# Optimization experiments

Measured on AMD Instinct MI355X. Metric: run time of the kernel, lower is better.

## Reference

```python
import jax, jax.numpy as jnp
import numpy as np

# ---- forest structure (static) ----
B = 32                      # number of trees in the batch
DEPTH = 12                  # topological levels per tree
LEVELS = [2 ** d for d in range(DEPTH)]           # nodes per level (root=level 0)
STARTS = np.concatenate([[0], np.cumsum(LEVELS)[:-1]]).astype(int)
NPG = int(sum(LEVELS))      # 4095 nodes per graph, node 0 = root
N = B * NPG                 # 131040 total nodes
VOCAB = 20000               # dataset.PAD_TOKEN_VALUE + 1
PAD = VOCAB - 1             # padding_idx
E = 256                     # embedding_dim (x_size)
H = 256                     # lstm_output_dim (h_size)
C = 104                     # num_classes (extra_non_linear=None)


def setup_inputs() -> dict:
    key = jax.random.key(0)
    ks = jax.random.split(key, 8)
    # random parent in the previous level for every non-root node (irregular fan-in)
    rng = np.random.RandomState(0)
    par = np.full(N, -1, dtype=np.int64)
    for g in range(B):
        off = g * NPG
        for d in range(1, DEPTH):
            nd = LEVELS[d]
            par[off + STARTS[d]: off + STARTS[d] + nd] = (
                off + STARTS[d - 1] + rng.randint(0, LEVELS[d - 1], size=nd))
    s = 0.05
    return {
        'x': jax.random.randint(ks[0], (N,), 0, VOCAB),
        'par': jnp.asarray(par),
        'emb': jax.random.normal(ks[1], (VOCAB, E), jnp.float32) * s,
        'W_iou': jax.random.normal(ks[2], (3 * H, E), jnp.float32) * s,
        'U_iou': jax.random.normal(ks[3], (3 * H, H), jnp.float32) * s,
        'b_iou': jnp.zeros((1, 3 * H), jnp.float32),
        'U_f_w': jax.random.normal(ks[4], (H, H), jnp.float32) * s,
        'U_f_b': jnp.zeros((H,), jnp.float32),
        'lin_w': jax.random.normal(ks[5], (C, H), jnp.float32) * s,
        'lin_b': jnp.zeros((C,), jnp.float32),
    }


def _forward(x, par, emb, W_iou, U_iou, b_iou, U_f_w, U_f_b, lin_w, lin_b):
    emb = emb.at[PAD].set(0.0)                 # padding_idx row is zero
    x_vec = emb[x]                             # [N, E]
    iou = x_vec @ W_iou.T                      # [N, 3H], W_iou has no bias
    h = jnp.zeros((N, H), x_vec.dtype)
    c = jnp.zeros((N, H), x_vec.dtype)
    offs = jnp.arange(B) * NPG
    # topological propagation: leaves (deepest level) -> root, per generation
    for d in range(DEPTH - 1, -1, -1):
        nd = LEVELS[d]
        nids = (offs[:, None] + STARTS[d] + jnp.arange(nd)).reshape(-1)  # [B*nd]
        iou_n = iou[nids]
        if d < DEPTH - 1:
            nc = LEVELS[d + 1]
            cids = (offs[:, None] + STARTS[d + 1] + jnp.arange(nc)).reshape(-1)
            h_ch = h[cids]                     # mailbox gather of child states
            c_ch = c[cids]
            p = par[cids]                      # global parent id per child
            seg = (p // NPG) * nd + (p % NPG - STARTS[d])  # parent slot in this level
            f = jax.nn.sigmoid(h_ch @ U_f_w.T + U_f_b)     # per-child forget gate
            h_tild = jax.ops.segment_sum(h_ch, seg, num_segments=B * nd)
            c_agg = jax.ops.segment_sum(f * c_ch, seg, num_segments=B * nd)
            iou_n = iou_n + h_tild @ U_iou.T
            c_n = c_agg
        else:
            c_n = jnp.zeros((B * nd, H), x_vec.dtype)
        iou_n = iou_n + b_iou
        i, o, u = jnp.split(iou_n, 3, axis=1)
        c_new = jax.nn.sigmoid(i) * jnp.tanh(u) + c_n
        h_new = jax.nn.sigmoid(o) * jnp.tanh(c_new)
        h = h.at[nids].set(h_new)
        c = c.at[nids].set(c_new)
    roots = h[offs]                            # graph.ndata['h'][0] per graph
    return roots @ lin_w.T + lin_b             # [B, num_classes]


def reference(x, par, emb, W_iou, U_iou, b_iou, U_f_w, U_f_b, lin_w, lin_b):
    return _forward(x, par, emb, W_iou, U_iou, b_iou, U_f_w, U_f_b, lin_w, lin_b)
```

## Files before the change

kernel.cpp:

```cpp
#include <hip/hip_runtime.h>
#include <hip/hip_bf16.h>


#define B_G     32
#define NPG     4095
#define NTOT    (B_G * NPG)
#define NCLS    104
#define VOCAB   20000
#define PAD_TOK 19999
#define KCAP    24
#define LB(d)   (32 * ((1 << (d)) - 1))

typedef unsigned short u16;
typedef unsigned int   u32;
typedef __attribute__((ext_vector_type(8))) short bfrag8;
typedef __attribute__((ext_vector_type(4))) float ffrag4;

__device__ __forceinline__ float bf2f(u16 v) {
    union { u32 u; float f; } x; x.u = ((u32)v) << 16; return x.f;
}
__device__ __forceinline__ u16 f2bf(float f) {
    union { __hip_bfloat16 h; u16 u; } c; c.h = __float2bfloat16(f); return c.u;
}
__device__ __forceinline__ float loadv(const void* b, int i, int isf32) {
    return isf32 ? ((const float*)b)[i] : bf2f(((const u16*)b)[i]);
}
__device__ __forceinline__ float sigf(float x) { return 1.f / (1.f + __expf(-x)); }

__global__ void probe_kernel(const void* emb, const void* Wiou, const void* Uiou,
                             const void* Ufw, const void* lw,
                             const int* x32, const int* par32, int* flags)
{
    if (threadIdx.x != 0 || blockIdx.x != 0) return;
    const void* ptrs[5] = { emb, Wiou, Uiou, Ufw, lw };
    for (int i = 0; i < 5; ++i) {
        const u16* p = (const u16*)ptrs[i];
        int big = 0;
        for (int k = 0; k < 128; ++k) {
            u32 e = (((u32)p[k]) << 16 >> 23) & 0xFF;
            if (e >= 129) ++big;
        }
        flags[i] = (big >= 4) ? 1 : 0;
    }
    int zx = 1;
    for (int k = 1; k <= 15; k += 2) if (x32[k] != 0) zx = 0;
    flags[5] = zx;
    flags[6] = (par32[3] == 0 && par32[5] == 0) ? 1 : 0;
}

__global__ __launch_bounds__(256) void prep_kernel(
    const int* __restrict__ x, const int* __restrict__ par,
    int* __restrict__ tokLvl, int* __restrict__ cnt, int* __restrict__ bucket,
    const int* __restrict__ flags)
{
    int gid = blockIdx.x * 256 + threadIdx.x;
    if (gid >= NTOT) return;
    int g     = (int)((u32)gid / NPG);
    int local = gid - g * NPG;
    int v  = local + 1;
    int d  = 31 - __clz(v);
    int j  = local - ((1 << d) - 1);
    int tok = flags[5] ? x[2 * gid] : x[gid];
    if (tok < 0 || tok >= VOCAB) tok = PAD_TOK;
    tokLvl[LB(d) + (g << d) + j] = tok;
    if (local > 0) {
        int p  = flags[6] ? par[2 * gid] : par[gid];
        p = max(0, min(p, NTOT - 1));
        int pg = (int)((u32)p / NPG);
        int pl = p - pg * NPG;
        int pd = d - 1;
        int ps = LB(pd) + (pg << pd) + (pl - ((1 << pd) - 1));
        ps = max(0, min(ps, 65503));
        int slot = atomicAdd(&cnt[ps], 1);
        if (slot < KCAP) bucket[(size_t)ps * KCAP + slot] = (g << d) + j;
    }
}

__global__ __launch_bounds__(256) void embconv_kernel(
    const void* __restrict__ emb, u16* __restrict__ embb,
    const int* __restrict__ flags)
{
    int i8 = (blockIdx.x * 256 + threadIdx.x) * 8;
    if (i8 >= VOCAB * 256) return;
    u16 v[8];
    if ((i8 >> 8) == PAD_TOK) {
        #pragma unroll
        for (int s = 0; s < 8; ++s) v[s] = 0;
    } else if (flags[0]) {
        const float* e = (const float*)emb + i8;
        float4 a = *(const float4*)e;
        float4 b = *(const float4*)(e + 4);
        v[0]=f2bf(a.x); v[1]=f2bf(a.y); v[2]=f2bf(a.z); v[3]=f2bf(a.w);
        v[4]=f2bf(b.x); v[5]=f2bf(b.y); v[6]=f2bf(b.z); v[7]=f2bf(b.w);
    } else {
        *(uint4*)v = *(const uint4*)((const u16*)emb + i8);
    }
    *(uint4*)(embb + i8) = *(uint4*)v;
}

__global__ __launch_bounds__(256) void wuc_kernel(
    const void* __restrict__ Wiou, const void* __restrict__ Uiou,
    u16* __restrict__ wuc, const int* __restrict__ flags)
{
    int idx = blockIdx.x * 256 + threadIdx.x;
    if (idx >= 16 * 768 * 32) return;
    int c   = idx / 24576;
    int rem = idx - c * 24576;
    int out = rem >> 5;
    int kk  = rem & 31;
    int k   = c * 32 + kk;
    float v = (k < 256) ? loadv(Wiou, out * 256 + k, flags[1])
                        : loadv(Uiou, out * 256 + (k - 256), flags[2]);
    wuc[idx] = f2bf(v);
}

__global__ __launch_bounds__(256) void ufc_kernel(
    const void* __restrict__ Ufw, u16* __restrict__ ufc,
    const int* __restrict__ flags)
{
    int idx = blockIdx.x * 256 + threadIdx.x;
    if (idx >= 8 * 256 * 32) return;
    int c   = idx >> 13;
    int rem = idx & 8191;
    int out = rem >> 5;
    int kk  = rem & 31;
    ufc[idx] = f2bf(loadv(Ufw, out * 256 + c * 32 + kk, flags[3]));
}

__global__ __launch_bounds__(256, 3) void gemm1_kernel(
    const u16* __restrict__ hch, u16* cbuf,
    const u16* __restrict__ ufc, const void* __restrict__ ufb,
    const int* __restrict__ flags)
{
    __shared__ u16 As[64][40];
    __shared__ u16 Bs[256][40];
    const int t = threadIdx.x;
    const int w = t >> 6, lane = t & 63, quad = lane >> 4, l15 = lane & 15;
    const int m0 = blockIdx.x * 64;
    const int f_uf = flags[3];

    ffrag4 acc[4][4];
    #pragma unroll
    for (int i = 0; i < 4; ++i)
        #pragma unroll
        for (int j = 0; j < 4; ++j) acc[i][j] = (ffrag4)0.f;

    const int arow = t >> 2, aseg = t & 3;
    for (int c = 0; c < 8; ++c) {
        *(uint4*)&As[arow][aseg * 8] =
            *(const uint4*)(hch + (size_t)(m0 + arow) * 256 + c * 32 + aseg * 8);
        #pragma unroll
        for (int r16 = 0; r16 < 4; ++r16) {
            int row = r16 * 64 + arow;
            *(uint4*)&Bs[row][aseg * 8] =
                *(const uint4*)(ufc + ((size_t)c * 256 + row) * 32 + aseg * 8);
        }
        __syncthreads();
        bfrag8 a[4], b[4];
        #pragma unroll
        for (int mt = 0; mt < 4; ++mt) a[mt] = *(bfrag8*)&As[mt * 16 + l15][quad * 8];
        #pragma unroll
        for (int nt = 0; nt < 4; ++nt) b[nt] = *(bfrag8*)&Bs[w * 64 + nt * 16 + l15][quad * 8];
        #pragma unroll
        for (int mt = 0; mt < 4; ++mt)
            #pragma unroll
            for (int nt = 0; nt < 4; ++nt)
                acc[mt][nt] = __builtin_amdgcn_mfma_f32_16x16x32_bf16(a[mt], b[nt], acc[mt][nt], 0, 0, 0);
        __syncthreads();
    }

    #pragma unroll
    for (int nt = 0; nt < 4; ++nt) {
        int hu = w * 64 + nt * 16 + l15;
        float fb = loadv(ufb, hu, f_uf);
        #pragma unroll
        for (int mt = 0; mt < 4; ++mt) {
            #pragma unroll
            for (int r = 0; r < 4; ++r) {
                int node = m0 + mt * 16 + quad * 4 + r;
                size_t off = (size_t)node * 256 + hu;
                float f = sigf(acc[mt][nt][r] + fb);
                cbuf[off] = f2bf(f * bf2f(cbuf[off]));
            }
        }
    }
}

__global__ __launch_bounds__(256) void agg_kernel(
    int NN, const u32* __restrict__ hch32, const u32* __restrict__ fcch32,
    const int* __restrict__ cnt_d, const int* __restrict__ bucket_d,
    u32* __restrict__ htild32, u32* __restrict__ cagg32)
{
    int pi  = blockIdx.x * 2 + (threadIdx.x >> 7);
    int col = threadIdx.x & 127;
    if (pi >= NN) return;
    int nc = min(cnt_d[pi], KCAP);
    float h0 = 0.f, h1 = 0.f, c0 = 0.f, c1 = 0.f;
    for (int ci = 0; ci < nc; ++ci) {
        int ch = bucket_d[(size_t)pi * KCAP + ci];
        u32 hv = hch32[(size_t)ch * 128 + col];
        u32 fv = fcch32[(size_t)ch * 128 + col];
        h0 += bf2f((u16)(hv & 0xffff)); h1 += bf2f((u16)(hv >> 16));
        c0 += bf2f((u16)(fv & 0xffff)); c1 += bf2f((u16)(fv >> 16));
    }
    htild32[(size_t)pi * 128 + col] = (u32)f2bf(h0) | ((u32)f2bf(h1) << 16);
    cagg32[(size_t)pi * 128 + col]  = (u32)f2bf(c0) | ((u32)f2bf(c1) << 16);
}

__global__ __launch_bounds__(256, 3) void gemm2_kernel(
    int nchunk, int NN,
    const int* __restrict__ tokLvl_d, const u16* __restrict__ embb,
    const u16* __restrict__ wuc, const void* __restrict__ biou,
    const u16* __restrict__ htild, const u16* __restrict__ cagg,
    u16* __restrict__ hdst, u16* __restrict__ cdst,
    const int* __restrict__ flags)
{
    __shared__ u16 As[128][40];
    __shared__ u16 Bs[192][40];
    __shared__ int toks[128];
    const int t = threadIdx.x;
    const int w = t >> 6, lane = t & 63, quad = lane >> 4, l15 = lane & 15;
    const int m0 = blockIdx.x * 128;
    const int q  = blockIdx.y;
    const int f_b = flags[1];

    if (t < 128) toks[t] = tokLvl_d[m0 + t];
    __syncthreads();

    ffrag4 acc[8][3];
    #pragma unroll
    for (int i = 0; i < 8; ++i)
        #pragma unroll
        for (int j = 0; j < 3; ++j) acc[i][j] = (ffrag4)0.f;

    const int arow = t >> 1, ac0 = (t & 1) * 16;
    const int brow = t >> 2, bseg = t & 3;
    for (int c = 0; c < nchunk; ++c) {
        if (c < 8) {
            const u16* e = embb + (size_t)toks[arow] * 256 + c * 32 + ac0;
            *(uint4*)&As[arow][ac0]     = *(const uint4*)e;
            *(uint4*)&As[arow][ac0 + 8] = *(const uint4*)(e + 8);
        } else {
            const u16* hsrc = htild + (size_t)(m0 + arow) * 256 + (c - 8) * 32 + ac0;
            *(uint4*)&As[arow][ac0]     = *(const uint4*)hsrc;
            *(uint4*)&As[arow][ac0 + 8] = *(const uint4*)(hsrc + 8);
        }
        #pragma unroll
        for (int g = 0; g < 3; ++g) {
            *(uint4*)&Bs[g * 64 + brow][bseg * 8] =
                *(const uint4*)(wuc + ((size_t)c * 768 + g * 256 + q * 64 + brow) * 32 + bseg * 8);
        }
        __syncthreads();
        bfrag8 a[8], b[3];
        #pragma unroll
        for (int mt = 0; mt < 8; ++mt) a[mt] = *(bfrag8*)&As[mt * 16 + l15][quad * 8];
        #pragma unroll
        for (int g = 0; g < 3; ++g) b[g] = *(bfrag8*)&Bs[g * 64 + w * 16 + l15][quad * 8];
        #pragma unroll
        for (int mt = 0; mt < 8; ++mt)
            #pragma unroll
            for (int g = 0; g < 3; ++g)
                acc[mt][g] = __builtin_amdgcn_mfma_f32_16x16x32_bf16(a[mt], b[g], acc[mt][g], 0, 0, 0);
        __syncthreads();
    }

    const int hu = q * 64 + w * 16 + l15;
    const float bi = loadv(biou, hu,       f_b);
    const float bo = loadv(biou, 256 + hu, f_b);
    const float bu = loadv(biou, 512 + hu, f_b);
    #pragma unroll
    for (int mt = 0; mt < 8; ++mt) {
        #pragma unroll
        for (int r = 0; r < 4; ++r) {
            int node = m0 + mt * 16 + quad * 4 + r;
            if (node < NN) {
                size_t off = (size_t)node * 256 + hu;
                float iv = acc[mt][0][r] + bi;
                float ov = acc[mt][1][r] + bo;
                float uv = acc[mt][2][r] + bu;
                float cg = cagg ? bf2f(cagg[off]) : 0.f;
                float cn = sigf(iv) * tanhf(uv) + cg;
                float hn = sigf(ov) * tanhf(cn);
                hdst[off] = f2bf(hn);
                cdst[off] = f2bf(cn);
            }
        }
    }
}

__global__ __launch_bounds__(1024, 1) void tail_kernel(
    const int* __restrict__ tokLvl, const u16* __restrict__ embb,
    const u16* __restrict__ wuc, const void* __restrict__ biou,
    const u16* __restrict__ ufc, const void* __restrict__ ufb,
    const u16* __restrict__ hB, const u16* __restrict__ cB,
    const int* __restrict__ cnt, const int* __restrict__ bucket,
    const void* __restrict__ lw, const void* __restrict__ lb,
    float* __restrict__ out, const int* __restrict__ flags)
{
    __shared__ u16 hs[64][264];
    __shared__ u16 cs[64][264];
    __shared__ u16 hts[32][264];
    __shared__ u16 cts[32][264];
    const int t = threadIdx.x;
    const int g = blockIdx.x;
    const int w = t >> 6;
    const int lane = t & 63, quad = lane >> 4, l15 = lane & 15;
    const int f_uf = flags[3], f_b = flags[1], f_lw = flags[4];

    #pragma unroll 1
    for (int i = t; i < 64 * 32; i += 1024) {
        int j = i >> 5, seg = i & 31;
        size_t off = (((size_t)((g << 6) + j)) << 8) + seg * 8;
        *(uint4*)&hs[j][seg * 8] = *(const uint4*)(hB + off);
        *(uint4*)&cs[j][seg * 8] = *(const uint4*)(cB + off);
    }
    __syncthreads();

    #pragma unroll 1
    for (int d = 5; d >= 0; --d) {
        const int ncr = 1 << (d + 1);
        const int np  = 1 << d;
        const int lvb = LB(d) + (g << d);
        const int hu  = w * 16 + l15;

        {
            ffrag4 facc[4];
            #pragma unroll
            for (int i = 0; i < 4; ++i) facc[i] = (ffrag4)0.f;
            #pragma unroll 2
            for (int c = 0; c < 8; ++c) {
                bfrag8 a[4];
                #pragma unroll
                for (int mt = 0; mt < 4; ++mt)
                    a[mt] = *(const bfrag8*)&hs[mt * 16 + l15][c * 32 + quad * 8];
                bfrag8 b = *(const bfrag8*)(ufc + ((size_t)c * 256 + w * 16 + l15) * 32 + quad * 8);
                #pragma unroll
                for (int mt = 0; mt < 4; ++mt)
                    facc[mt] = __builtin_amdgcn_mfma_f32_16x16x32_bf16(a[mt], b, facc[mt], 0, 0, 0);
            }
            float fb = loadv(ufb, hu, f_uf);
            #pragma unroll
            for (int mt = 0; mt < 4; ++mt) {
                #pragma unroll
                for (int r = 0; r < 4; ++r) {
                    int j = mt * 16 + quad * 4 + r;
                    if (j < ncr) {
                        float f = sigf(facc[mt][r] + fb);
                        cs[j][hu] = f2bf(f * bf2f(cs[j][hu]));
                    }
                }
            }
        }
        __syncthreads();

        {
            const int col = t & 127;
            #pragma unroll 1
            for (int pi = t >> 7; pi < np; pi += 8) {
                int nc = min(cnt[lvb + pi], KCAP);
                const int* bk = bucket + (size_t)(lvb + pi) * KCAP;
                float h0 = 0.f, h1 = 0.f, c0 = 0.f, c1 = 0.f;
                #pragma unroll 1
                for (int ci = 0; ci < nc; ++ci) {
                    int j = bk[ci] & (ncr - 1);
                    u32 hv = *(const u32*)&hs[j][col * 2];
                    u32 cv = *(const u32*)&cs[j][col * 2];
                    h0 += bf2f((u16)(hv & 0xffff)); h1 += bf2f((u16)(hv >> 16));
                    c0 += bf2f((u16)(cv & 0xffff)); c1 += bf2f((u16)(cv >> 16));
                }
                *(u32*)&hts[pi][col * 2] = (u32)f2bf(h0) | ((u32)f2bf(h1) << 16);
                *(u32*)&cts[pi][col * 2] = (u32)f2bf(c0) | ((u32)f2bf(c1) << 16);
            }
        }
        __syncthreads();

        {
            int tok0 = tokLvl[lvb + min(l15, np - 1)];
            int tok1 = tokLvl[lvb + min(16 + l15, np - 1)];
            ffrag4 acc[2][3];
            #pragma unroll
            for (int i = 0; i < 2; ++i)
                #pragma unroll
                for (int j = 0; j < 3; ++j) acc[i][j] = (ffrag4)0.f;
            #pragma unroll 2
            for (int c = 0; c < 16; ++c) {
                bfrag8 a0, a1;
                if (c < 8) {
                    a0 = *(const bfrag8*)(embb + (size_t)tok0 * 256 + c * 32 + quad * 8);
                    a1 = *(const bfrag8*)(embb + (size_t)tok1 * 256 + c * 32 + quad * 8);
                } else {
                    a0 = *(const bfrag8*)&hts[l15][(c - 8) * 32 + quad * 8];
                    a1 = *(const bfrag8*)&hts[16 + l15][(c - 8) * 32 + quad * 8];
                }
                #pragma unroll
                for (int g3 = 0; g3 < 3; ++g3) {
                    bfrag8 b = *(const bfrag8*)(wuc + ((size_t)c * 768 + g3 * 256 + w * 16 + l15) * 32 + quad * 8);
                    acc[0][g3] = __builtin_amdgcn_mfma_f32_16x16x32_bf16(a0, b, acc[0][g3], 0, 0, 0);
                    acc[1][g3] = __builtin_amdgcn_mfma_f32_16x16x32_bf16(a1, b, acc[1][g3], 0, 0, 0);
                }
            }
            float bi = loadv(biou, hu,       f_b);
            float bo = loadv(biou, 256 + hu, f_b);
            float bu = loadv(biou, 512 + hu, f_b);
            #pragma unroll
            for (int mt = 0; mt < 2; ++mt) {
                #pragma unroll
                for (int r = 0; r < 4; ++r) {
                    int p = mt * 16 + quad * 4 + r;
                    if (p < np) {
                        float iv = acc[mt][0][r] + bi;
                        float ov = acc[mt][1][r] + bo;
                        float uv = acc[mt][2][r] + bu;
                        float cn = sigf(iv) * tanhf(uv) + bf2f(cts[p][hu]);
                        float hn = sigf(ov) * tanhf(cn);
                        hs[p][hu] = f2bf(hn);
                        cs[p][hu] = f2bf(cn);
                    }
                }
            }
        }
        __syncthreads();
    }

    if (t < NCLS) {
        float acc = 0.f;
        #pragma unroll 1
        for (int k = 0; k < 256; ++k)
            acc += loadv(lw, t * 256 + k, f_lw) * bf2f(hs[0][k]);
        out[(size_t)g * NCLS + t] = acc + loadv(lb, t, f_lw);
    }
}

__global__ void fill_kernel(float* out, int n, float v) {
    int i = blockIdx.x * 256 + threadIdx.x;
    if (i < n) out[i] = v;
}

extern "C" void kernel_launch(void* const* d_in, const int* in_sizes, int n_in,
                              void* d_out, int out_size, void* d_ws, size_t ws_size,
                              hipStream_t stream)
{
    float* out = (float*)d_out;

    static const int exp_sizes[10] = {131040, 131040, 5120000, 196608, 196608,
                                      768, 65536, 256, 26624, 104};
    bool shapes_ok = (n_in == 10) && (out_size == B_G * NCLS);
    for (int i = 0; i < 10 && shapes_ok; ++i)
        if (in_sizes[i] != exp_sizes[i]) shapes_ok = false;
    if (!shapes_ok) {
        fill_kernel<<<(out_size + 255) / 256, 256, 0, stream>>>(out, out_size, 2.0f);
        return;
    }

    const int* x     = (const int*)d_in[0];
    const int* par   = (const int*)d_in[1];
    const void* emb  = d_in[2];
    const void* Wiou = d_in[3];
    const void* Uiou = d_in[4];
    const void* biou = d_in[5];
    const void* Ufw  = d_in[6];
    const void* Ufb  = d_in[7];
    const void* lw   = d_in[8];
    const void* lb   = d_in[9];

    char* W = (char*)d_ws;
    u16* hA     = (u16*)(W + 0);
    u16* hB     = (u16*)(W + 33554432);
    u16* cA     = (u16*)(W + 50331648);
    u16* cB     = (u16*)(W + 83886080);
    u16* htild  = (u16*)(W + 100663296);
    u16* cagg   = (u16*)(W + 117440512);
    u16* WUc    = (u16*)(W + 134217728);
    u16* Ufc    = (u16*)(W + 135004160);
    int* tokLvl = (int*)(W + 135135232);
    int* cnt    = (int*)(W + 135659520);
    int* bucket = (int*)(W + 135921664);
    u16* embb   = (u16*)(W + 142213120);
    int* flags  = (int*)(W + 152453120);
    const size_t NEED = 152453184;
    if (ws_size < NEED) {
        fill_kernel<<<(out_size + 255) / 256, 256, 0, stream>>>(out, out_size, 1.0f);
        return;
    }

    hipMemsetAsync(cnt, 0, 65536 * sizeof(int), stream);
    probe_kernel<<<1, 1, 0, stream>>>(emb, Wiou, Uiou, Ufw, lw, x, par, flags);
    prep_kernel<<<(NTOT + 255) / 256, 256, 0, stream>>>(x, par, tokLvl, cnt, bucket, flags);
    embconv_kernel<<<2500, 256, 0, stream>>>(emb, embb, flags);
    wuc_kernel<<<1536, 256, 0, stream>>>(Wiou, Uiou, WUc, flags);
    ufc_kernel<<<256, 256, 0, stream>>>(Ufw, Ufc, flags);

    gemm2_kernel<<<dim3(512, 4), 256, 0, stream>>>(
        8, 65536, tokLvl + LB(11), embb, WUc, biou,
        nullptr, nullptr, hA, cA, flags);

    for (int d = 10; d >= 6; --d) {
        const int cl = d + 1;
        const int NC = B_G << cl;
        const int NN = B_G << d;
        const u16* hch = (cl & 1) ? hA : hB;
        u16*       cch = (cl & 1) ? cA : cB;
        u16* hdst = (d & 1) ? hA : hB;
        u16* cdst = (d & 1) ? cA : cB;
        gemm1_kernel<<<NC / 64, 256, 0, stream>>>(hch, cch, Ufc, Ufb, flags);
        agg_kernel<<<(NN + 1) / 2, 256, 0, stream>>>(
            NN, (const u32*)hch, (const u32*)cch,
            cnt + LB(d), bucket + (size_t)LB(d) * KCAP,
            (u32*)htild, (u32*)cagg);
        gemm2_kernel<<<dim3((NN + 127) / 128, 4), 256, 0, stream>>>(
            16, NN, tokLvl + LB(d), embb, WUc, biou,
            htild, cagg, hdst, cdst, flags);
    }

    tail_kernel<<<B_G, 1024, 0, stream>>>(
        tokLvl, embb, WUc, biou, Ufc, Ufb,
        hB, cB, cnt, bucket, lw, lb, out, flags);
}
```

Measured before the change: 704.9 us.

## Parallelize probe, merge conversion kernels, stage GEMM epilogues through LDS

```diff
diff --git a/kernel.cpp b/kernel.cpp
--- a/kernel.cpp
+++ b/kernel.cpp
@@ -11,6 +11,12 @@
 #define KCAP    24
 #define LB(d)   (32 * ((1 << (d)) - 1))
 
+#define EMB_BLKS  2500
+#define WUC_BLKS  1536
+#define UFC_BLKS  256
+#define PREP_BLKS 512
+#define CONV_BLKS (EMB_BLKS + WUC_BLKS + UFC_BLKS + PREP_BLKS)
+
 typedef unsigned short u16;
 typedef unsigned int   u32;
 typedef __attribute__((ext_vector_type(8))) short bfrag8;
@@ -27,104 +33,105 @@
 }
 __device__ __forceinline__ float sigf(float x) { return 1.f / (1.f + __expf(-x)); }
 
-__global__ void probe_kernel(const void* emb, const void* Wiou, const void* Uiou,
-                             const void* Ufw, const void* lw,
-                             const int* x32, const int* par32, int* flags)
-{
-    if (threadIdx.x != 0 || blockIdx.x != 0) return;
+__global__ __launch_bounds__(384) void probe_kernel(
+    const void* emb, const void* Wiou, const void* Uiou,
+    const void* Ufw, const void* lw,
+    const int* x32, const int* par32, int* flags)
+{
+    if (blockIdx.x != 0) return;
+    const int w = threadIdx.x >> 6, lane = threadIdx.x & 63;
     const void* ptrs[5] = { emb, Wiou, Uiou, Ufw, lw };
-    for (int i = 0; i < 5; ++i) {
-        const u16* p = (const u16*)ptrs[i];
+    if (w < 5) {
+        const u16* p = (const u16*)ptrs[w];
         int big = 0;
-        for (int k = 0; k < 128; ++k) {
-            u32 e = (((u32)p[k]) << 16 >> 23) & 0xFF;
+        #pragma unroll
+        for (int k = 0; k < 2; ++k) {
+            u32 e = (((u32)p[lane * 2 + k]) << 16 >> 23) & 0xFF;
             if (e >= 129) ++big;
         }
-        flags[i] = (big >= 4) ? 1 : 0;
-    }
-    int zx = 1;
-    for (int k = 1; k <= 15; k += 2) if (x32[k] != 0) zx = 0;
-    flags[5] = zx;
-    flags[6] = (par32[3] == 0 && par32[5] == 0) ? 1 : 0;
-}
-
-__global__ __launch_bounds__(256) void prep_kernel(
+        unsigned long long m1 = __ballot(big >= 1);
+        unsigned long long m2 = __ballot(big >= 2);
+        int tot = __popcll(m1) + __popcll(m2);
+        if (lane == 0) flags[w] = (tot >= 4) ? 1 : 0;
+    } else if (w == 5) {
+        int bad = (lane < 8) ? (x32[2 * lane + 1] != 0) : 0;
+        unsigned long long mx = __ballot(bad != 0);
+        if (lane == 0) {
+            flags[5] = (mx == 0) ? 1 : 0;
+            flags[6] = (par32[3] == 0 && par32[5] == 0) ? 1 : 0;
+        }
+    }
+}
+
+__global__ __launch_bounds__(256) void convert_kernel(
+    const void* __restrict__ emb, u16* __restrict__ embb,
+    const void* __restrict__ Wiou, const void* __restrict__ Uiou,
+    u16* __restrict__ wuc,
+    const void* __restrict__ Ufw, u16* __restrict__ ufc,
     const int* __restrict__ x, const int* __restrict__ par,
     int* __restrict__ tokLvl, int* __restrict__ cnt, int* __restrict__ bucket,
     const int* __restrict__ flags)
 {
-    int gid = blockIdx.x * 256 + threadIdx.x;
-    if (gid >= NTOT) return;
-    int g     = (int)((u32)gid / NPG);
-    int local = gid - g * NPG;
-    int v  = local + 1;
-    int d  = 31 - __clz(v);
-    int j  = local - ((1 << d) - 1);
-    int tok = flags[5] ? x[2 * gid] : x[gid];
-    if (tok < 0 || tok >= VOCAB) tok = PAD_TOK;
-    tokLvl[LB(d) + (g << d) + j] = tok;
-    if (local > 0) {
-        int p  = flags[6] ? par[2 * gid] : par[gid];
-        p = max(0, min(p, NTOT - 1));
-        int pg = (int)((u32)p / NPG);
-        int pl = p - pg * NPG;
-        int pd = d - 1;
-        int ps = LB(pd) + (pg << pd) + (pl - ((1 << pd) - 1));
-        ps = max(0, min(ps, 65503));
-        int slot = atomicAdd(&cnt[ps], 1);
-        if (slot < KCAP) bucket[(size_t)ps * KCAP + slot] = (g << d) + j;
-    }
-}
-
-__global__ __launch_bounds__(256) void embconv_kernel(
-    const void* __restrict__ emb, u16* __restrict__ embb,
-    const int* __restrict__ flags)
-{
-    int i8 = (blockIdx.x * 256 + threadIdx.x) * 8;
-    if (i8 >= VOCAB * 256) return;
-    u16 v[8];
-    if ((i8 >> 8) == PAD_TOK) {
-        #pragma unroll
-        for (int s = 0; s < 8; ++s) v[s] = 0;
-    } else if (flags[0]) {
-        const float* e = (const float*)emb + i8;
-        float4 a = *(const float4*)e;
-        float4 b = *(const float4*)(e + 4);
-        v[0]=f2bf(a.x); v[1]=f2bf(a.y); v[2]=f2bf(a.z); v[3]=f2bf(a.w);
-        v[4]=f2bf(b.x); v[5]=f2bf(b.y); v[6]=f2bf(b.z); v[7]=f2bf(b.w);
+    const int b = blockIdx.x;
+    if (b < EMB_BLKS) {
+        int i8 = (b * 256 + (int)threadIdx.x) * 8;
+        if (i8 >= VOCAB * 256) return;
+        u16 v[8];
+        if ((i8 >> 8) == PAD_TOK) {
+            #pragma unroll
+            for (int s = 0; s < 8; ++s) v[s] = 0;
+        } else if (flags[0]) {
+            const float* e = (const float*)emb + i8;
+            float4 a = *(const float4*)e;
+            float4 c = *(const float4*)(e + 4);
+            v[0]=f2bf(a.x); v[1]=f2bf(a.y); v[2]=f2bf(a.z); v[3]=f2bf(a.w);
+            v[4]=f2bf(c.x); v[5]=f2bf(c.y); v[6]=f2bf(c.z); v[7]=f2bf(c.w);
+        } else {
+            *(uint4*)v = *(const uint4*)((const u16*)emb + i8);
+        }
+        *(uint4*)(embb + i8) = *(uint4*)v;
+    } else if (b < EMB_BLKS + WUC_BLKS) {
+        int idx = (b - EMB_BLKS) * 256 + (int)threadIdx.x;
+        if (idx >= 16 * 768 * 32) return;
+        int c   = idx / 24576;
+        int rem = idx - c * 24576;
+        int out = rem >> 5;
+        int kk  = rem & 31;
+        int k   = c * 32 + kk;
+        float v = (k < 256) ? loadv(Wiou, out * 256 + k, flags[1])
+                            : loadv(Uiou, out * 256 + (k - 256), flags[2]);
+        wuc[idx] = f2bf(v);
+    } else if (b < EMB_BLKS + WUC_BLKS + UFC_BLKS) {
+        int idx = (b - EMB_BLKS - WUC_BLKS) * 256 + (int)threadIdx.x;
+        if (idx >= 8 * 256 * 32) return;
+        int c   = idx >> 13;
+        int rem = idx & 8191;
+        int out = rem >> 5;
+        int kk  = rem & 31;
+        ufc[idx] = f2bf(loadv(Ufw, out * 256 + c * 32 + kk, flags[3]));
     } else {
-        *(uint4*)v = *(const uint4*)((const u16*)emb + i8);
-    }
-    *(uint4*)(embb + i8) = *(uint4*)v;
-}
-
-__global__ __launch_bounds__(256) void wuc_kernel(
-    const void* __restrict__ Wiou, const void* __restrict__ Uiou,
-    u16* __restrict__ wuc, const int* __restrict__ flags)
-{
-    int idx = blockIdx.x * 256 + threadIdx.x;
-    if (idx >= 16 * 768 * 32) return;
-    int c   = idx / 24576;
-    int rem = idx - c * 24576;
-    int out = rem >> 5;
-    int kk  = rem & 31;
-    int k   = c * 32 + kk;
-    float v = (k < 256) ? loadv(Wiou, out * 256 + k, flags[1])
-                        : loadv(Uiou, out * 256 + (k - 256), flags[2]);
-    wuc[idx] = f2bf(v);
-}
-
-__global__ __launch_bounds__(256) void ufc_kernel(
-    const void* __restrict__ Ufw, u16* __restrict__ ufc,
-    const int* __restrict__ flags)
-{
-    int idx = blockIdx.x * 256 + threadIdx.x;
-    if (idx >= 8 * 256 * 32) return;
-    int c   = idx >> 13;
-    int rem = idx & 8191;
-    int out = rem >> 5;
-    int kk  = rem & 31;
-    ufc[idx] = f2bf(loadv(Ufw, out * 256 + c * 32 + kk, flags[3]));
+        int gid = (b - EMB_BLKS - WUC_BLKS - UFC_BLKS) * 256 + (int)threadIdx.x;
+        if (gid >= NTOT) return;
+        int g     = (int)((u32)gid / NPG);
+        int local = gid - g * NPG;
+        int v  = local + 1;
+        int d  = 31 - __clz(v);
+        int j  = local - ((1 << d) - 1);
+        int tok = flags[5] ? x[2 * gid] : x[gid];
+        if (tok < 0 || tok >= VOCAB) tok = PAD_TOK;
+        tokLvl[LB(d) + (g << d) + j] = tok;
+        if (local > 0) {
+            int p  = flags[6] ? par[2 * gid] : par[gid];
+            p = max(0, min(p, NTOT - 1));
+            int pg = (int)((u32)p / NPG);
+            int pl = p - pg * NPG;
+            int pd = d - 1;
+            int ps = LB(pd) + (pg << pd) + (pl - ((1 << pd) - 1));
+            ps = max(0, min(ps, 65503));
+            int slot = atomicAdd(&cnt[ps], 1);
+            if (slot < KCAP) bucket[(size_t)ps * KCAP + slot] = (g << d) + j;
+        }
+    }
 }
 
 __global__ __launch_bounds__(256, 3) void gemm1_kernel(
@@ -132,8 +139,13 @@
     const u16* __restrict__ ufc, const void* __restrict__ ufb,
     const int* __restrict__ flags)
 {
-    __shared__ u16 As[64][40];
-    __shared__ u16 Bs[256][40];
+    __shared__ union {
+        struct { u16 As[64][40]; u16 Bs[256][40]; } k;
+        u16 tile[64][264];
+    } sm;
+    auto& As = sm.k.As;
+    auto& Bs = sm.k.Bs;
+    auto& tile = sm.tile;
     const int t = threadIdx.x;
     const int w = t >> 6, lane = t & 63, quad = lane >> 4, l15 = lane & 15;
     const int m0 = blockIdx.x * 64;
@@ -169,6 +181,13 @@
         __syncthreads();
     }
 
+    const int srow = t >> 2, sseg = t & 3;
+    const size_t sgb = (size_t)(m0 + srow) * 256 + sseg * 64;
+    #pragma unroll
+    for (int k = 0; k < 8; ++k)
+        *(uint4*)&tile[srow][sseg * 64 + k * 8] = *(const uint4*)(cbuf + sgb + k * 8);
+    __syncthreads();
+
     #pragma unroll
     for (int nt = 0; nt < 4; ++nt) {
         int hu = w * 64 + nt * 16 + l15;
@@ -177,13 +196,16 @@
         for (int mt = 0; mt < 4; ++mt) {
             #pragma unroll
             for (int r = 0; r < 4; ++r) {
-                int node = m0 + mt * 16 + quad * 4 + r;
-                size_t off = (size_t)node * 256 + hu;
+                int row = mt * 16 + quad * 4 + r;
                 float f = sigf(acc[mt][nt][r] + fb);
-                cbuf[off] = f2bf(f * bf2f(cbuf[off]));
+                tile[row][hu] = f2bf(f * bf2f(tile[row][hu]));
             }
         }
     }
+    __syncthreads();
+    #pragma unroll
+    for (int k = 0; k < 8; ++k)
+        *(uint4*)(cbuf + sgb + k * 8) = *(const uint4*)&tile[srow][sseg * 64 + k * 8];
 }
 
 __global__ __launch_bounds__(256) void agg_kernel(
@@ -215,9 +237,14 @@
     u16* __restrict__ hdst, u16* __restrict__ cdst,
     const int* __restrict__ flags)
 {
-    __shared__ u16 As[128][40];
-    __shared__ u16 Bs[192][40];
+    __shared__ union {
+        struct { u16 As[128][40]; u16 Bs[192][40]; } k;
+        u16 tile[128][72];
+    } sm;
     __shared__ int toks[128];
+    auto& As = sm.k.As;
+    auto& Bs = sm.k.Bs;
+    auto& tile = sm.tile;
     const int t = threadIdx.x;
     const int w = t >> 6, lane = t & 63, quad = lane >> 4, l15 = lane & 15;
     const int m0 = blockIdx.x * 128;
@@ -264,27 +291,59 @@
         __syncthreads();
     }
 
-    const int hu = q * 64 + w * 16 + l15;
+    const int hu  = q * 64 + w * 16 + l15;
+    const int huL = w * 16 + l15;
     const float bi = loadv(biou, hu,       f_b);
     const float bo = loadv(biou, 256 + hu, f_b);
     const float bu = loadv(biou, 512 + hu, f_b);
+
+    const int srow = t >> 1, sseg = t & 1;
+    const size_t sgbase = (size_t)(m0 + srow) * 256 + q * 64 + sseg * 32;
+    const bool svalid = (m0 + srow) < NN;
+
+    if (cagg) {
+        if (svalid) {
+            #pragma unroll
+            for (int k = 0; k < 4; ++k)
+                *(uint4*)&tile[srow][sseg * 32 + k * 8] =
+                    *(const uint4*)(cagg + sgbase + k * 8);
+        }
+    }
+    __syncthreads();
+
+    u16 cnv[8][4];
     #pragma unroll
     for (int mt = 0; mt < 8; ++mt) {
         #pragma unroll
         for (int r = 0; r < 4; ++r) {
-            int node = m0 + mt * 16 + quad * 4 + r;
-            if (node < NN) {
-                size_t off = (size_t)node * 256 + hu;
-                float iv = acc[mt][0][r] + bi;
-                float ov = acc[mt][1][r] + bo;
-                float uv = acc[mt][2][r] + bu;
-                float cg = cagg ? bf2f(cagg[off]) : 0.f;
-                float cn = sigf(iv) * tanhf(uv) + cg;
-                float hn = sigf(ov) * tanhf(cn);
-                hdst[off] = f2bf(hn);
-                cdst[off] = f2bf(cn);
-            }
-        }
+            int row = mt * 16 + quad * 4 + r;
+            float cg = cagg ? bf2f(tile[row][huL]) : 0.f;
+            float iv = acc[mt][0][r] + bi;
+            float ov = acc[mt][1][r] + bo;
+            float uv = acc[mt][2][r] + bu;
+            float cn = sigf(iv) * tanhf(uv) + cg;
+            float hn = sigf(ov) * tanhf(cn);
+            cnv[mt][r] = f2bf(cn);
+            tile[row][huL] = f2bf(hn);
+        }
+    }
+    __syncthreads();
+    if (svalid) {
+        #pragma unroll
+        for (int k = 0; k < 4; ++k)
+            *(uint4*)(hdst + sgbase + k * 8) = *(const uint4*)&tile[srow][sseg * 32 + k * 8];
+    }
+    __syncthreads();
+    #pragma unroll
+    for (int mt = 0; mt < 8; ++mt)
+        #pragma unroll
+        for (int r = 0; r < 4; ++r)
+            tile[mt * 16 + quad * 4 + r][huL] = cnv[mt][r];
+    __syncthreads();
+    if (svalid) {
+        #pragma unroll
+        for (int k = 0; k < 4; ++k)
+            *(uint4*)(cdst + sgbase + k * 8) = *(const uint4*)&tile[srow][sseg * 32 + k * 8];
     }
 }
 
@@ -484,11 +543,10 @@
     }
 
     hipMemsetAsync(cnt, 0, 65536 * sizeof(int), stream);
-    probe_kernel<<<1, 1, 0, stream>>>(emb, Wiou, Uiou, Ufw, lw, x, par, flags);
-    prep_kernel<<<(NTOT + 255) / 256, 256, 0, stream>>>(x, par, tokLvl, cnt, bucket, flags);
-    embconv_kernel<<<2500, 256, 0, stream>>>(emb, embb, flags);
-    wuc_kernel<<<1536, 256, 0, stream>>>(Wiou, Uiou, WUc, flags);
-    ufc_kernel<<<256, 256, 0, stream>>>(Ufw, Ufc, flags);
+    probe_kernel<<<1, 384, 0, stream>>>(emb, Wiou, Uiou, Ufw, lw, x, par, flags);
+    convert_kernel<<<CONV_BLKS, 256, 0, stream>>>(
+        emb, embb, Wiou, Uiou, WUc, Ufw, Ufc,
+        x, par, tokLvl, cnt, bucket, flags);
 
     gemm2_kernel<<<dim3(512, 4), 256, 0, stream>>>(
         8, 65536, tokLvl + LB(11), embb, WUc, biou,
```

After: 647.6 us. 1.09x faster.
